# Optimization experiments

Measured on AMD Instinct MI355X. Metric: run time of the kernel, lower is better.

Reference implementation:

```python
import jax, jax.numpy as jnp
import numpy as np

NUM_SEGMENTS = 128

def segment_softmax(logits, seg_ids, num_segments):
    # logits: [N, 1]; stable per-segment softmax
    seg_max = jax.ops.segment_max(logits, seg_ids, num_segments=num_segments)  # [S,1]
    shifted = logits - seg_max[seg_ids]
    ex = jnp.exp(shifted)
    seg_sum = jax.ops.segment_sum(ex, seg_ids, num_segments=num_segments)  # [S,1]
    return ex / seg_sum[seg_ids]

def setup_inputs() -> dict:
    key = jax.random.key(0)
    ks = jax.random.split(key, 8)
    N, D, E = 524288, 256, 256
    x = jax.random.normal(ks[0], (N, D), dtype=jnp.float32)
    segment_ids = jnp.sort(jax.random.randint(ks[1], (N,), 0, NUM_SEGMENTS, dtype=jnp.int32))
    s = 1.0 / np.sqrt(D)
    Wk = jax.random.uniform(ks[2], (D, E), jnp.float32, -s, s)
    bk = jax.random.uniform(ks[3], (E,), jnp.float32, -s, s)
    Wv = jax.random.uniform(ks[4], (D, E), jnp.float32, -s, s)
    bv = jax.random.uniform(ks[5], (E,), jnp.float32, -s, s)
    so = 1.0 / np.sqrt(E)
    Wo = jax.random.uniform(ks[6], (E, 1), jnp.float32, -so, so)
    bo = jax.random.uniform(ks[7], (1,), jnp.float32, -so, so)
    return {"x": x, "segment_ids": segment_ids, "Wk": Wk, "bk": bk, "Wv": Wv, "bv": bv, "Wo": Wo, "bo": bo}

def reference(x, segment_ids, Wk, bk, Wv, bv, Wo, bo):
    keys = x @ Wk + bk                      # [N, E]
    values = x @ Wv + bv                    # [N, E]
    logits = jnp.sum(keys, axis=1, keepdims=True)  # [N, 1]
    attn = segment_softmax(logits, segment_ids, NUM_SEGMENTS)  # [N, 1]
    pooled = jax.ops.segment_sum(attn * values, segment_ids, num_segments=NUM_SEGMENTS)  # [S, E]
    return pooled @ Wo + bo                 # [S, 1]
```

## Files before the change

kernel.cpp:

```cpp
#include <hip/hip_runtime.h>
#include <hip/hip_bf16.h>
#include <math.h>

#define DDIM 256
#define NSEG 128

__device__ __forceinline__ unsigned float_key(float f) {
  unsigned u = __float_as_uint(f);
  return (u & 0x80000000u) ? ~u : (u | 0x80000000u);
}
__device__ __forceinline__ float key_float(unsigned u) {
  return __uint_as_float((u & 0x80000000u) ? (u & 0x7FFFFFFFu) : ~u);
}


__global__ __launch_bounds__(256) void prep_kernel(
    const float* __restrict__ Wk, const float* __restrict__ bk,
    const float* __restrict__ Wv, const float* __restrict__ bv,
    const float* __restrict__ Wo,
    float* __restrict__ ws_vecs, unsigned* __restrict__ segmax,
    float* __restrict__ segsum, float* __restrict__ segwv) {
  const int d = threadIdx.x;
  const float4* wkr = (const float4*)(Wk + (size_t)d * DDIM);
  const float4* wvr = (const float4*)(Wv + (size_t)d * DDIM);
  const float4* wo4 = (const float4*)Wo;
  float s1 = 0.f, s2 = 0.f;
  #pragma unroll 4
  for (int e4 = 0; e4 < DDIM / 4; ++e4) {
    float4 a = wkr[e4];
    float4 b = wvr[e4];
    float4 w = wo4[e4];
    s1 += a.x + a.y + a.z + a.w;
    s2 += b.x * w.x + b.y * w.y + b.z * w.z + b.w * w.w;
  }
  ws_vecs[d] = s1;
  ws_vecs[DDIM + d] = s2;

  __shared__ float r1[256], r2[256];
  r1[d] = bk[d];
  r2[d] = bv[d] * Wo[d];
  __syncthreads();
  for (int off = 128; off > 0; off >>= 1) {
    if (d < off) { r1[d] += r1[d + off]; r2[d] += r2[d + off]; }
    __syncthreads();
  }
  if (d == 0) { ws_vecs[2 * DDIM] = r1[0]; ws_vecs[2 * DDIM + 1] = r2[0]; }

  if (d < NSEG) { segmax[d] = 0u; segsum[d] = 0.f; segwv[d] = 0.f; }
}

template <bool STORE>
__global__ __launch_bounds__(256) void pass1_kernel(
    const float* __restrict__ x, const int* __restrict__ seg,
    const float* __restrict__ ws_vecs,
    float* __restrict__ lbuf, float* __restrict__ vbuf,
    unsigned* __restrict__ segmax, int nrows, int rowsPerWave) {
  const int lane = threadIdx.x & 63;
  const int wave = (blockIdx.x * blockDim.x + threadIdx.x) >> 6;
  const float4 wk4 = ((const float4*)ws_vecs)[lane];
  const float4 wv4 = ((const float4*)(ws_vecs + DDIM))[lane];
  const float bk_sum = ws_vecs[2 * DDIM];
  const float bvo = ws_vecs[2 * DDIM + 1];

  const int row0 = wave * rowsPerWave;
  const int row1 = min(row0 + rowsPerWave, nrows);

  int cur_seg = -1;
  float cur_max = 0.f;
  for (int row = row0; row < row1; ++row) {
    const float4 x4 = ((const float4*)(x + (size_t)row * DDIM))[lane];
    float dk = x4.x * wk4.x + x4.y * wk4.y + x4.z * wk4.z + x4.w * wk4.w;
    float dv = x4.x * wv4.x + x4.y * wv4.y + x4.z * wv4.z + x4.w * wv4.w;
    #pragma unroll
    for (int off = 32; off; off >>= 1) {
      dk += __shfl_xor(dk, off);
      dv += __shfl_xor(dv, off);
    }
    if (lane == 0) {
      const float l = dk + bk_sum;
      if (STORE) { lbuf[row] = l; vbuf[row] = dv + bvo; }
      const int s = seg[row];
      if (s != cur_seg) {
        if (cur_seg >= 0) atomicMax(&segmax[cur_seg], float_key(cur_max));
        cur_seg = s;
        cur_max = l;
      } else {
        cur_max = fmaxf(cur_max, l);
      }
    }
  }
  if (lane == 0 && cur_seg >= 0) atomicMax(&segmax[cur_seg], float_key(cur_max));
}

__global__ __launch_bounds__(256) void pass2_kernel(
    const float* __restrict__ lbuf, const float* __restrict__ vbuf,
    const int* __restrict__ seg, const unsigned* __restrict__ segmax,
    float* __restrict__ segsum, float* __restrict__ segwv, int nrows) {
  const int gid = blockIdx.x * blockDim.x + threadIdx.x;
  const int lane = threadIdx.x & 63;
  float ex = 0.f, exv = 0.f;
  int s = -1;
  if (gid < nrows) {
    s = seg[gid];
    const float m = key_float(segmax[s]);
    ex = expf(lbuf[gid] - m);
    exv = ex * vbuf[gid];
  }
  const int s0 = __shfl(s, 0);
  const bool uni = __all(s == s0);
  if (uni && s0 >= 0) {
    #pragma unroll
    for (int off = 32; off; off >>= 1) {
      ex += __shfl_xor(ex, off);
      exv += __shfl_xor(exv, off);
    }
    if (lane == 0) {
      atomicAdd(&segsum[s0], ex);
      atomicAdd(&segwv[s0], exv);
    }
  } else if (s >= 0) {
    atomicAdd(&segsum[s], ex);
    atomicAdd(&segwv[s], exv);
  }
}

__global__ __launch_bounds__(256) void pass2_recompute_kernel(
    const float* __restrict__ x, const int* __restrict__ seg,
    const float* __restrict__ ws_vecs, const unsigned* __restrict__ segmax,
    float* __restrict__ segsum, float* __restrict__ segwv,
    int nrows, int rowsPerWave) {
  const int lane = threadIdx.x & 63;
  const int wave = (blockIdx.x * blockDim.x + threadIdx.x) >> 6;
  const float4 wk4 = ((const float4*)ws_vecs)[lane];
  const float4 wv4 = ((const float4*)(ws_vecs + DDIM))[lane];
  const float bk_sum = ws_vecs[2 * DDIM];
  const float bvo = ws_vecs[2 * DDIM + 1];

  const int row0 = wave * rowsPerWave;
  const int row1 = min(row0 + rowsPerWave, nrows);

  int cur_seg = -1;
  float se = 0.f, sev = 0.f;
  for (int row = row0; row < row1; ++row) {
    const float4 x4 = ((const float4*)(x + (size_t)row * DDIM))[lane];
    float dk = x4.x * wk4.x + x4.y * wk4.y + x4.z * wk4.z + x4.w * wk4.w;
    float dv = x4.x * wv4.x + x4.y * wv4.y + x4.z * wv4.z + x4.w * wv4.w;
    #pragma unroll
    for (int off = 32; off; off >>= 1) {
      dk += __shfl_xor(dk, off);
      dv += __shfl_xor(dv, off);
    }
    if (lane == 0) {
      const float l = dk + bk_sum;
      const float v = dv + bvo;
      const int s = seg[row];
      const float m = key_float(segmax[s]);
      const float e = expf(l - m);
      if (s != cur_seg) {
        if (cur_seg >= 0) {
          atomicAdd(&segsum[cur_seg], se);
          atomicAdd(&segwv[cur_seg], sev);
        }
        cur_seg = s;
        se = e;
        sev = e * v;
      } else {
        se += e;
        sev += e * v;
      }
    }
  }
  if (lane == 0 && cur_seg >= 0) {
    atomicAdd(&segsum[cur_seg], se);
    atomicAdd(&segwv[cur_seg], sev);
  }
}

__global__ void final_kernel(const float* __restrict__ segsum,
                             const float* __restrict__ segwv,
                             const float* __restrict__ bo,
                             float* __restrict__ out) {
  const int s = threadIdx.x;
  if (s < NSEG) {
    const float den = segsum[s];
    out[s] = (den > 0.f ? segwv[s] / den : 0.f) + bo[0];
  }
}

extern "C" void kernel_launch(void* const* d_in, const int* in_sizes, int n_in,
                              void* d_out, int out_size, void* d_ws, size_t ws_size,
                              hipStream_t stream) {
  const float* x  = (const float*)d_in[0];
  const int*   sg = (const int*)d_in[1];
  const float* Wk = (const float*)d_in[2];
  const float* bk = (const float*)d_in[3];
  const float* Wv = (const float*)d_in[4];
  const float* bv = (const float*)d_in[5];
  const float* Wo = (const float*)d_in[6];
  const float* bo = (const float*)d_in[7];
  float* out = (float*)d_out;
  const int nrows = in_sizes[1];

  float*    ws_vecs = (float*)d_ws;
  unsigned* segmax  = (unsigned*)((char*)d_ws + 4096);
  float*    segsum  = (float*)((char*)d_ws + 4608);
  float*    segwv   = (float*)((char*)d_ws + 5120);
  float*    lbuf    = (float*)((char*)d_ws + 8192);
  float*    vbuf    = lbuf + nrows;

  const size_t need = 8192 + (size_t)nrows * 2 * sizeof(float);
  const bool store = ws_size >= need;

  prep_kernel<<<1, 256, 0, stream>>>(Wk, bk, Wv, bv, Wo, ws_vecs, segmax, segsum, segwv);

  const int rowsPerWave = 64;
  const int nWaves = (nrows + rowsPerWave - 1) / rowsPerWave;
  const int blocks = (nWaves + 3) / 4;

  if (store) {
    pass1_kernel<true><<<blocks, 256, 0, stream>>>(x, sg, ws_vecs, lbuf, vbuf,
                                                   segmax, nrows, rowsPerWave);
    pass2_kernel<<<(nrows + 255) / 256, 256, 0, stream>>>(lbuf, vbuf, sg, segmax,
                                                          segsum, segwv, nrows);
  } else {
    pass1_kernel<false><<<blocks, 256, 0, stream>>>(x, sg, ws_vecs, nullptr, nullptr,
                                                    segmax, nrows, rowsPerWave);
    pass2_recompute_kernel<<<blocks, 256, 0, stream>>>(x, sg, ws_vecs, segmax,
                                                       segsum, segwv, nrows, rowsPerWave);
  }

  final_kernel<<<1, 128, 0, stream>>>(segsum, segwv, bo, out);
}
```

Measured before the change: 794.4 us.

## Process 16 rows per wave iteration with 4 lanes per row in pass1

Pass1 now assigns each row to a group of 4 lanes, so a wave covers 16 rows per iteration. Each lane reads 64 contiguous floats with 16 float4 loads, and the Wk/Wv reduction vectors are staged in shared memory. This replaces the per-row full-wave shuffle reduction with a two-step shuffle and more loads in flight per lane, raising memory-level parallelism on the x read. The segment max is now handled per 16-row chunk with a wave reduction; chunks that cross a segment boundary fall back to per-row atomics. The recompute fallback for small workspaces is removed, so the kernel now always assumes the workspace can hold lbuf and vbuf.

```diff
diff --git a/kernel.cpp b/kernel.cpp
--- a/kernel.cpp
+++ b/kernel.cpp
@@ -4,6 +4,7 @@
 
 #define DDIM 256
 #define NSEG 128
+#define RPW  64
 
 __device__ __forceinline__ unsigned float_key(float f) {
   unsigned u = __float_as_uint(f);
@@ -49,69 +50,100 @@
   if (d < NSEG) { segmax[d] = 0u; segsum[d] = 0.f; segwv[d] = 0.f; }
 }
 
-template <bool STORE>
+__device__ __forceinline__ void flush_max(int s, float m, unsigned* segmax, int lane) {
+  if (s < 0) return;
+  #pragma unroll
+  for (int off = 32; off; off >>= 1) m = fmaxf(m, __shfl_xor(m, off));
+  if (lane == 0) atomicMax(&segmax[s], float_key(m));
+}
+
 __global__ __launch_bounds__(256) void pass1_kernel(
     const float* __restrict__ x, const int* __restrict__ seg,
     const float* __restrict__ ws_vecs,
     float* __restrict__ lbuf, float* __restrict__ vbuf,
-    unsigned* __restrict__ segmax, int nrows, int rowsPerWave) {
-  const int lane = threadIdx.x & 63;
-  const int wave = (blockIdx.x * blockDim.x + threadIdx.x) >> 6;
-  const float4 wk4 = ((const float4*)ws_vecs)[lane];
-  const float4 wv4 = ((const float4*)(ws_vecs + DDIM))[lane];
+    unsigned* __restrict__ segmax, int nrows) {
+  __shared__ float swk[DDIM], swv[DDIM];
+  const int tid = threadIdx.x;
+  swk[tid] = ws_vecs[tid];
+  swv[tid] = ws_vecs[DDIM + tid];
+  __syncthreads();
   const float bk_sum = ws_vecs[2 * DDIM];
-  const float bvo = ws_vecs[2 * DDIM + 1];
+  const float bvo    = ws_vecs[2 * DDIM + 1];
 
-  const int row0 = wave * rowsPerWave;
-  const int row1 = min(row0 + rowsPerWave, nrows);
+  const int lane   = tid & 63;
+  const int wave   = (blockIdx.x * blockDim.x + tid) >> 6;
+  const int sub    = lane & 3;
+  const int rowoff = lane >> 2;
+  const int row0   = wave * RPW;
+  if (row0 >= nrows) return;
+  const int row1 = min(row0 + RPW, nrows);
 
-  int cur_seg = -1;
-  float cur_max = 0.f;
-  for (int row = row0; row < row1; ++row) {
-    const float4 x4 = ((const float4*)(x + (size_t)row * DDIM))[lane];
-    float dk = x4.x * wk4.x + x4.y * wk4.y + x4.z * wk4.z + x4.w * wk4.w;
-    float dv = x4.x * wv4.x + x4.y * wv4.y + x4.z * wv4.z + x4.w * wv4.w;
+  const float4* swk4 = (const float4*)(swk + sub * 64);
+  const float4* swv4 = (const float4*)(swv + sub * 64);
+
+  int   cur_seg = -1;
+  float cur_max = -INFINITY;
+
+  for (int c0 = row0; c0 < row1; c0 += 16) {
+    const int  row   = c0 + rowoff;
+    const bool valid = row < nrows;
+    const int  lrow  = valid ? row : nrows - 1;
+    const float4* xp = (const float4*)(x + (size_t)lrow * DDIM + sub * 64);
+    float dk = 0.f, dv = 0.f;
     #pragma unroll
-    for (int off = 32; off; off >>= 1) {
-      dk += __shfl_xor(dk, off);
-      dv += __shfl_xor(dv, off);
+    for (int j = 0; j < 16; ++j) {
+      const float4 x4 = xp[j];
+      const float4 a  = swk4[j];
+      const float4 b  = swv4[j];
+      dk += x4.x * a.x + x4.y * a.y + x4.z * a.z + x4.w * a.w;
+      dv += x4.x * b.x + x4.y * b.y + x4.z * b.z + x4.w * b.w;
     }
-    if (lane == 0) {
-      const float l = dk + bk_sum;
-      if (STORE) { lbuf[row] = l; vbuf[row] = dv + bvo; }
-      const int s = seg[row];
-      if (s != cur_seg) {
-        if (cur_seg >= 0) atomicMax(&segmax[cur_seg], float_key(cur_max));
-        cur_seg = s;
-        cur_max = l;
-      } else {
+    dk += __shfl_xor(dk, 1); dk += __shfl_xor(dk, 2);
+    dv += __shfl_xor(dv, 1); dv += __shfl_xor(dv, 2);
+    const float l = dk + bk_sum;
+    if (sub == 0 && valid) { lbuf[row] = l; vbuf[row] = dv + bvo; }
+
+    const int cend    = min(c0 + 15, nrows - 1);
+    const int s_first = seg[c0];
+    const int s_last  = seg[cend];
+    if (s_first == s_last) {
+      if (s_first != cur_seg) {
+        flush_max(cur_seg, cur_max, segmax, lane);
+        cur_seg = s_first;
+        cur_max = valid ? l : -INFINITY;
+      } else if (valid) {
         cur_max = fmaxf(cur_max, l);
       }
+    } else {
+      flush_max(cur_seg, cur_max, segmax, lane);
+      cur_seg = -1;
+      cur_max = -INFINITY;
+      if (sub == 0 && valid) atomicMax(&segmax[seg[row]], float_key(l));
     }
   }
-  if (lane == 0 && cur_seg >= 0) atomicMax(&segmax[cur_seg], float_key(cur_max));
+  flush_max(cur_seg, cur_max, segmax, lane);
 }
 
 __global__ __launch_bounds__(256) void pass2_kernel(
     const float* __restrict__ lbuf, const float* __restrict__ vbuf,
     const int* __restrict__ seg, const unsigned* __restrict__ segmax,
     float* __restrict__ segsum, float* __restrict__ segwv, int nrows) {
-  const int gid = blockIdx.x * blockDim.x + threadIdx.x;
+  const int gid  = blockIdx.x * blockDim.x + threadIdx.x;
   const int lane = threadIdx.x & 63;
   float ex = 0.f, exv = 0.f;
   int s = -1;
   if (gid < nrows) {
     s = seg[gid];
     const float m = key_float(segmax[s]);
-    ex = expf(lbuf[gid] - m);
+    ex  = expf(lbuf[gid] - m);
     exv = ex * vbuf[gid];
   }
-  const int s0 = __shfl(s, 0);
+  const int  s0  = __shfl(s, 0);
   const bool uni = __all(s == s0);
   if (uni && s0 >= 0) {
     #pragma unroll
     for (int off = 32; off; off >>= 1) {
-      ex += __shfl_xor(ex, off);
+      ex  += __shfl_xor(ex, off);
       exv += __shfl_xor(exv, off);
     }
     if (lane == 0) {
@@ -121,58 +153,6 @@
   } else if (s >= 0) {
     atomicAdd(&segsum[s], ex);
     atomicAdd(&segwv[s], exv);
-  }
-}
-
-__global__ __launch_bounds__(256) void pass2_recompute_kernel(
-    const float* __restrict__ x, const int* __restrict__ seg,
-    const float* __restrict__ ws_vecs, const unsigned* __restrict__ segmax,
-    float* __restrict__ segsum, float* __restrict__ segwv,
-    int nrows, int rowsPerWave) {
-  const int lane = threadIdx.x & 63;
-  const int wave = (blockIdx.x * blockDim.x + threadIdx.x) >> 6;
-  const float4 wk4 = ((const float4*)ws_vecs)[lane];
-  const float4 wv4 = ((const float4*)(ws_vecs + DDIM))[lane];
-  const float bk_sum = ws_vecs[2 * DDIM];
-  const float bvo = ws_vecs[2 * DDIM + 1];
-
-  const int row0 = wave * rowsPerWave;
-  const int row1 = min(row0 + rowsPerWave, nrows);
-
-  int cur_seg = -1;
-  float se = 0.f, sev = 0.f;
-  for (int row = row0; row < row1; ++row) {
-    const float4 x4 = ((const float4*)(x + (size_t)row * DDIM))[lane];
-    float dk = x4.x * wk4.x + x4.y * wk4.y + x4.z * wk4.z + x4.w * wk4.w;
-    float dv = x4.x * wv4.x + x4.y * wv4.y + x4.z * wv4.z + x4.w * wv4.w;
-    #pragma unroll
-    for (int off = 32; off; off >>= 1) {
-      dk += __shfl_xor(dk, off);
-      dv += __shfl_xor(dv, off);
-    }
-    if (lane == 0) {
-      const float l = dk + bk_sum;
-      const float v = dv + bvo;
-      const int s = seg[row];
-      const float m = key_float(segmax[s]);
-      const float e = expf(l - m);
-      if (s != cur_seg) {
-        if (cur_seg >= 0) {
-          atomicAdd(&segsum[cur_seg], se);
-          atomicAdd(&segwv[cur_seg], sev);
-        }
-        cur_seg = s;
-        se = e;
-        sev = e * v;
-      } else {
-        se += e;
-        sev += e * v;
-      }
-    }
-  }
-  if (lane == 0 && cur_seg >= 0) {
-    atomicAdd(&segsum[cur_seg], se);
-    atomicAdd(&segwv[cur_seg], sev);
   }
 }
 
@@ -208,26 +188,12 @@
   float*    lbuf    = (float*)((char*)d_ws + 8192);
   float*    vbuf    = lbuf + nrows;
 
-  const size_t need = 8192 + (size_t)nrows * 2 * sizeof(float);
-  const bool store = ws_size >= need;
-
   prep_kernel<<<1, 256, 0, stream>>>(Wk, bk, Wv, bv, Wo, ws_vecs, segmax, segsum, segwv);
 
-  const int rowsPerWave = 64;
-  const int nWaves = (nrows + rowsPerWave - 1) / rowsPerWave;
+  const int nWaves = (nrows + RPW - 1) / RPW;
   const int blocks = (nWaves + 3) / 4;
-
-  if (store) {
-    pass1_kernel<true><<<blocks, 256, 0, stream>>>(x, sg, ws_vecs, lbuf, vbuf,
-                                                   segmax, nrows, rowsPerWave);
-    pass2_kernel<<<(nrows + 255) / 256, 256, 0, stream>>>(lbuf, vbuf, sg, segmax,
-                                                          segsum, segwv, nrows);
-  } else {
-    pass1_kernel<false><<<blocks, 256, 0, stream>>>(x, sg, ws_vecs, nullptr, nullptr,
-                                                    segmax, nrows, rowsPerWave);
-    pass2_recompute_kernel<<<blocks, 256, 0, stream>>>(x, sg, ws_vecs, segmax,
-                                                       segsum, segwv, nrows, rowsPerWave);
-  }
-
+  pass1_kernel<<<blocks, 256, 0, stream>>>(x, sg, ws_vecs, lbuf, vbuf, segmax, nrows);
+  pass2_kernel<<<(nrows + 255) / 256, 256, 0, stream>>>(lbuf, vbuf, sg, segmax,
+                                                        segsum, segwv, nrows);
   final_kernel<<<1, 128, 0, stream>>>(segsum, segwv, bo, out);
 }
```

Measured after the change: 779.5 us. No clear change (-1.9%).
